# Performance work log

Measured on AMD Instinct MI355X. Metric: run time of the kernel, lower is better.

Reference implementation:

```python
import jax, jax.numpy as jnp
import numpy as np

G = 128        # grid resolution per axis (points are voxel centers on this grid)
N = 262144     # number of input points == number of output points
CIN = 16
COUT = 32


def _build_neighbors(inp_coords, out_coords):
    """Emulates FixedRadiusSearch(Linf, r=1.53*voxel) + invert_neighbors_list on a
    unit grid: for each output point and each of the 27 kernel taps t, find the
    (unique) input point at out_coord - (t-1), or -1 if that voxel is empty."""
    enc = lambda c: (c[:, 0].astype(np.int64) * G + c[:, 1]) * G + c[:, 2]
    inp_keys = enc(inp_coords)
    order = np.argsort(inp_keys)
    skeys = inp_keys[order]
    nbr = np.full((out_coords.shape[0], 27), -1, dtype=np.int32)
    k = 0
    for t0 in range(3):
        for t1 in range(3):
            for t2 in range(3):
                d = np.array([t0 - 1, t1 - 1, t2 - 1], dtype=np.int64)
                nc = out_coords - d  # input voxel s.t. (out - inp) == d
                valid = np.all((nc >= 0) & (nc < G), axis=1)
                keys = enc(np.clip(nc, 0, G - 1))
                pos = np.searchsorted(skeys, keys).clip(0, len(skeys) - 1)
                found = valid & (skeys[pos] == keys)
                nbr[:, k] = np.where(found, order[pos].astype(np.int32), -1)
                k += 1
    return nbr


def setup_inputs() -> dict:
    rng = np.random.default_rng(0)
    # unique voxels -> at most one point per voxel (regular-grid assumption)
    inp_keys = rng.choice(G ** 3, size=N, replace=False)
    out_keys = rng.choice(G ** 3, size=N, replace=False)
    dec = lambda kk: np.stack([kk // (G * G), (kk // G) % G, kk % G], axis=1).astype(np.int64)
    nbr_idx = jnp.asarray(_build_neighbors(dec(inp_keys), dec(out_keys)))

    key = jax.random.key(0)
    k1, k2 = jax.random.split(key)
    inp_features = jax.random.normal(k1, (N, CIN), dtype=jnp.float32)
    # matches kernel_initializer = uniform_(-0.05, 0.05)
    kernel = jax.random.uniform(k2, (3, 3, 3, CIN, COUT), dtype=jnp.float32,
                                minval=-0.05, maxval=0.05)
    bias = jnp.zeros((COUT,), dtype=jnp.float32)  # bias_initializer = zeros_
    return {"inp_features": inp_features, "kernel": kernel, "bias": bias,
            "nbr_idx": nbr_idx}


def reference(inp_features, kernel, bias, nbr_idx):
    # continuous_conv_transpose with interpolation='nearest_neighbor',
    # coordinate_mapping='identity', normalize=False on a unit grid:
    # out[j] = sum_t W[t] @ f[nbr(j, t)]  (missing taps contribute zero), + bias
    valid = (nbr_idx >= 0)
    idx = jnp.where(valid, nbr_idx, 0)
    gathered = inp_features[idx] * valid[..., None].astype(inp_features.dtype)  # [N,27,Cin]
    W = kernel.reshape(27, kernel.shape[-2], kernel.shape[-1])                  # [27,Cin,Cout]
    return jnp.einsum('nkc,kco->no', gathered, W) + bias
```

## Files before the change

### kernel.cpp

```cpp
#include <hip/hip_runtime.h>
#include <hip/hip_bf16.h>

#define NPTS  262144
#define CIN   16
#define COUT  32
#define NTAPS 27
#define BLK   512
#define DEPTH 12

typedef __attribute__((ext_vector_type(8)))  short short8v;
typedef __attribute__((ext_vector_type(16))) float f32x16;

__global__ __launch_bounds__(256) void cvt_feat_kernel(
    const float* __restrict__ feat, __hip_bfloat16* __restrict__ fb)
{
    const int i = blockIdx.x * 256 + threadIdx.x;
    const float4 x = ((const float4*)feat)[i];
    __hip_bfloat162* o = (__hip_bfloat162*)fb;
    o[2 * i]     = __float22bfloat162_rn(float2{x.x, x.y});
    o[2 * i + 1] = __float22bfloat162_rn(float2{x.z, x.w});
}

template<bool USE_WS>
__global__ __launch_bounds__(BLK, 3) void sct_mfma_kernel(
    const float* __restrict__ feat,
    const __hip_bfloat16* __restrict__ featb,
    const float* __restrict__ Wg,
    const float* __restrict__ bias,
    const int*   __restrict__ nbr,
    float*       __restrict__ out)
{
    __shared__ short bpack[NTAPS * 512];

    const int tid = threadIdx.x;
    for (int i = tid; i < NTAPS * 512; i += BLK) {
        const int tap  = i >> 9;
        const int r    = i & 511;
        const int ln   = r >> 3;
        const int e    = r & 7;
        const int cin  = ((ln >> 5) << 3) + e;
        const int cout = ln & 31;
        const __hip_bfloat16 h = __float2bfloat16(Wg[(tap * CIN + cin) * COUT + cout]);
        bpack[i] = *(const short*)&h;
    }
    __syncthreads();

    const int lane = tid & 63;
    const int wv   = tid >> 6;
    const int p0   = blockIdx.x * 256 + wv * 32;
    const int prow = lane & 31;
    const int g    = lane >> 5;
    const int* nb  = nbr + (long)(p0 + prow) * NTAPS;

    int nid[NTAPS];
    #pragma unroll
    for (int q = 0; q < 6; ++q) {
        const int4 v = *(const int4*)(nb + 4 * q);
        nid[4*q+0] = v.x; nid[4*q+1] = v.y; nid[4*q+2] = v.z; nid[4*q+3] = v.w;
    }
    {
        const int2 v2 = *(const int2*)(nb + 24);
        nid[24] = v2.x; nid[25] = v2.y; nid[26] = nb[26];
    }

    f32x16 acc;
    {
        const float b = bias[prow];
        #pragma unroll
        for (int r2 = 0; r2 < 16; ++r2) acc[r2] = b;
    }

    short8v af[DEPTH];

    auto gather1 = [&](int t, short8v& dst) {
        const int id = nid[t];
        short8v a = {};
        if (id >= 0) {
            if (USE_WS) {
                a = *(const short8v*)(featb + (long)id * CIN + g * 8);
            } else {
                const float4* fp = (const float4*)(feat + (long)id * CIN + g * 8);
                const float4 x = fp[0];
                const float4 y = fp[1];
                union { short8v v; __hip_bfloat162 h[4]; } u;
                u.h[0] = __float22bfloat162_rn(float2{x.x, x.y});
                u.h[1] = __float22bfloat162_rn(float2{x.z, x.w});
                u.h[2] = __float22bfloat162_rn(float2{y.x, y.y});
                u.h[3] = __float22bfloat162_rn(float2{y.z, y.w});
                a = u.v;
            }
        }
        dst = a;
    };

    #pragma unroll
    for (int t = 0; t < DEPTH; ++t) gather1(t, af[t]);

    #pragma unroll
    for (int t = 0; t < NTAPS; ++t) {
        const short8v bf = *(const short8v*)&bpack[(t << 9) + (lane << 3)];
        acc = __builtin_amdgcn_mfma_f32_32x32x16_bf16(af[t % DEPTH], bf, acc, 0, 0, 0);
        if (t + DEPTH < NTAPS) gather1(t + DEPTH, af[(t + DEPTH) % DEPTH]);
    }

    #pragma unroll
    for (int r2 = 0; r2 < 16; ++r2) {
        const int row = (r2 & 3) + 8 * (r2 >> 2) + 4 * g;
        out[(long)(p0 + row) * COUT + prow] = acc[r2];
    }
}

extern "C" void kernel_launch(void* const* d_in, const int* in_sizes, int n_in,
                              void* d_out, int out_size, void* d_ws, size_t ws_size,
                              hipStream_t stream) {
    const float* feat = (const float*)d_in[0];
    const float* Wg   = (const float*)d_in[1];
    const float* bias = (const float*)d_in[2];
    const int*   nbr  = (const int*)d_in[3];
    float*       out  = (float*)d_out;

    const size_t need = (size_t)NPTS * CIN * sizeof(__hip_bfloat16);
    if (ws_size >= need) {
        __hip_bfloat16* fb = (__hip_bfloat16*)d_ws;
        cvt_feat_kernel<<<NPTS * CIN / 4 / 256, 256, 0, stream>>>(feat, fb);
        sct_mfma_kernel<true><<<NPTS / 256, BLK, 0, stream>>>(feat, fb, Wg, bias, nbr, out);
    } else {
        sct_mfma_kernel<false><<<NPTS / 256, BLK, 0, stream>>>(feat, nullptr, Wg, bias, nbr, out);
    }
}
```

Before: 43.86 us.

## Drop bf16 pre-conversion kernel, gather fp32 directly with streaming tap loop

Removes the separate fp32-to-bf16 feature conversion kernel and its launch, converting gathered fp32 features inline instead. The 12-deep register prefetch ring and the up-front 27-index load are replaced by loading neighbor indices in groups of four with nontemporal loads and issuing each tap's gather and MFMA together, with occupancy raised to 4 blocks per CU. Weight packing into LDS now uses vectorized float4 reads, and outputs use nontemporal stores. Gathers now read twice as many bytes per tap, and the explicit software pipelining is given up in favor of more resident waves to hide latency.

```diff
diff --git a/kernel.cpp b/kernel.cpp
--- a/kernel.cpp
+++ b/kernel.cpp
@@ -6,25 +6,13 @@
 #define COUT  32
 #define NTAPS 27
 #define BLK   512
-#define DEPTH 12
 
 typedef __attribute__((ext_vector_type(8)))  short short8v;
 typedef __attribute__((ext_vector_type(16))) float f32x16;
+typedef __attribute__((ext_vector_type(4)))  int   int4v;
 
-__global__ __launch_bounds__(256) void cvt_feat_kernel(
-    const float* __restrict__ feat, __hip_bfloat16* __restrict__ fb)
-{
-    const int i = blockIdx.x * 256 + threadIdx.x;
-    const float4 x = ((const float4*)feat)[i];
-    __hip_bfloat162* o = (__hip_bfloat162*)fb;
-    o[2 * i]     = __float22bfloat162_rn(float2{x.x, x.y});
-    o[2 * i + 1] = __float22bfloat162_rn(float2{x.z, x.w});
-}
-
-template<bool USE_WS>
-__global__ __launch_bounds__(BLK, 3) void sct_mfma_kernel(
+__global__ __launch_bounds__(BLK, 4) void sct_mfma_kernel(
     const float* __restrict__ feat,
-    const __hip_bfloat16* __restrict__ featb,
     const float* __restrict__ Wg,
     const float* __restrict__ bias,
     const int*   __restrict__ nbr,
@@ -33,15 +21,25 @@
     __shared__ short bpack[NTAPS * 512];
 
     const int tid = threadIdx.x;
-    for (int i = tid; i < NTAPS * 512; i += BLK) {
-        const int tap  = i >> 9;
-        const int r    = i & 511;
-        const int ln   = r >> 3;
-        const int e    = r & 7;
-        const int cin  = ((ln >> 5) << 3) + e;
-        const int cout = ln & 31;
-        const __hip_bfloat16 h = __float2bfloat16(Wg[(tap * CIN + cin) * COUT + cout]);
-        bpack[i] = *(const short*)&h;
+    #pragma unroll
+    for (int q = 0; q < 7; ++q) {
+        const int f = tid + q * BLK;
+        if (f < 3456) {
+            const float4 w4 = ((const float4*)Wg)[f];
+            const int tap = f >> 7;
+            const int r   = f & 127;
+            const int cin = r >> 3;
+            const int c0  = (r & 7) * 4;
+            const int base = (tap << 9) + ((cin >> 3) << 8) + (cin & 7);
+            const __hip_bfloat16 h0 = __float2bfloat16(w4.x);
+            const __hip_bfloat16 h1 = __float2bfloat16(w4.y);
+            const __hip_bfloat16 h2 = __float2bfloat16(w4.z);
+            const __hip_bfloat16 h3 = __float2bfloat16(w4.w);
+            bpack[base + (c0 + 0) * 8] = *(const short*)&h0;
+            bpack[base + (c0 + 1) * 8] = *(const short*)&h1;
+            bpack[base + (c0 + 2) * 8] = *(const short*)&h2;
+            bpack[base + (c0 + 3) * 8] = *(const short*)&h3;
+        }
     }
     __syncthreads();
 
@@ -52,17 +50,6 @@
     const int g    = lane >> 5;
     const int* nb  = nbr + (long)(p0 + prow) * NTAPS;
 
-    int nid[NTAPS];
-    #pragma unroll
-    for (int q = 0; q < 6; ++q) {
-        const int4 v = *(const int4*)(nb + 4 * q);
-        nid[4*q+0] = v.x; nid[4*q+1] = v.y; nid[4*q+2] = v.z; nid[4*q+3] = v.w;
-    }
-    {
-        const int2 v2 = *(const int2*)(nb + 24);
-        nid[24] = v2.x; nid[25] = v2.y; nid[26] = nb[26];
-    }
-
     f32x16 acc;
     {
         const float b = bias[prow];
@@ -70,43 +57,44 @@
         for (int r2 = 0; r2 < 16; ++r2) acc[r2] = b;
     }
 
-    short8v af[DEPTH];
-
-    auto gather1 = [&](int t, short8v& dst) {
-        const int id = nid[t];
+    auto tap1 = [&](int t, int id) {
         short8v a = {};
         if (id >= 0) {
-            if (USE_WS) {
-                a = *(const short8v*)(featb + (long)id * CIN + g * 8);
-            } else {
-                const float4* fp = (const float4*)(feat + (long)id * CIN + g * 8);
-                const float4 x = fp[0];
-                const float4 y = fp[1];
-                union { short8v v; __hip_bfloat162 h[4]; } u;
-                u.h[0] = __float22bfloat162_rn(float2{x.x, x.y});
-                u.h[1] = __float22bfloat162_rn(float2{x.z, x.w});
-                u.h[2] = __float22bfloat162_rn(float2{y.x, y.y});
-                u.h[3] = __float22bfloat162_rn(float2{y.z, y.w});
-                a = u.v;
-            }
+            const float4* fp = (const float4*)(feat + (long)id * CIN + g * 8);
+            const float4 x = fp[0];
+            const float4 y = fp[1];
+            union { short8v v; __hip_bfloat162 h[4]; } u;
+            u.h[0] = __float22bfloat162_rn(float2{x.x, x.y});
+            u.h[1] = __float22bfloat162_rn(float2{x.z, x.w});
+            u.h[2] = __float22bfloat162_rn(float2{y.x, y.y});
+            u.h[3] = __float22bfloat162_rn(float2{y.z, y.w});
+            a = u.v;
         }
-        dst = a;
+        const short8v bf = *(const short8v*)&bpack[(t << 9) + (lane << 3)];
+        acc = __builtin_amdgcn_mfma_f32_32x32x16_bf16(a, bf, acc, 0, 0, 0);
     };
 
     #pragma unroll
-    for (int t = 0; t < DEPTH; ++t) gather1(t, af[t]);
-
-    #pragma unroll
-    for (int t = 0; t < NTAPS; ++t) {
-        const short8v bf = *(const short8v*)&bpack[(t << 9) + (lane << 3)];
-        acc = __builtin_amdgcn_mfma_f32_32x32x16_bf16(af[t % DEPTH], bf, acc, 0, 0, 0);
-        if (t + DEPTH < NTAPS) gather1(t + DEPTH, af[(t + DEPTH) % DEPTH]);
+    for (int grp = 0; grp < 6; ++grp) {
+        const int4v v = __builtin_nontemporal_load((const int4v*)(nb + 4 * grp));
+        tap1(4 * grp + 0, v.x);
+        tap1(4 * grp + 1, v.y);
+        tap1(4 * grp + 2, v.z);
+        tap1(4 * grp + 3, v.w);
+    }
+    {
+        const int i24 = __builtin_nontemporal_load(nb + 24);
+        const int i25 = __builtin_nontemporal_load(nb + 25);
+        const int i26 = __builtin_nontemporal_load(nb + 26);
+        tap1(24, i24);
+        tap1(25, i25);
+        tap1(26, i26);
     }
 
     #pragma unroll
     for (int r2 = 0; r2 < 16; ++r2) {
         const int row = (r2 & 3) + 8 * (r2 >> 2) + 4 * g;
-        out[(long)(p0 + row) * COUT + prow] = acc[r2];
+        __builtin_nontemporal_store(acc[r2], &out[(long)(p0 + row) * COUT + prow]);
     }
 }
 
@@ -119,12 +107,5 @@
     const int*   nbr  = (const int*)d_in[3];
     float*       out  = (float*)d_out;
 
-    const size_t need = (size_t)NPTS * CIN * sizeof(__hip_bfloat16);
-    if (ws_size >= need) {
-        __hip_bfloat16* fb = (__hip_bfloat16*)d_ws;
-        cvt_feat_kernel<<<NPTS * CIN / 4 / 256, 256, 0, stream>>>(feat, fb);
-        sct_mfma_kernel<true><<<NPTS / 256, BLK, 0, stream>>>(feat, fb, Wg, bias, nbr, out);
-    } else {
-        sct_mfma_kernel<false><<<NPTS / 256, BLK, 0, stream>>>(feat, nullptr, Wg, bias, nbr, out);
-    }
+    sct_mfma_kernel<<<NPTS / 256, BLK, 0, stream>>>(feat, Wg, bias, nbr, out);
 }
```

Measured after the change: 54.73 us. 1.25x slower.
